# Performance work log

Hardware: AMD Instinct MI355X
Metric: run time of the kernel (lower is better)

Reference implementation:

```python
import jax, jax.numpy as jnp
import numpy as np


def _pad_reflect_br(x):
    # kornia filter2d with a 2x2 kernel pads (0 before, 1 after) in H and W, reflect mode
    return jnp.pad(x, ((0, 1), (0, 1)), mode='reflect')


def _gx(img):
    # correlation with [[-1,1],[-1,1]] at 'same' positions (pad after only)
    p = _pad_reflect_br(img)
    return -p[:-1, :-1] + p[:-1, 1:] - p[1:, :-1] + p[1:, 1:]


def _gy(img):
    # correlation with [[-1,-1],[1,1]]
    p = _pad_reflect_br(img)
    return -p[:-1, :-1] - p[:-1, 1:] + p[1:, :-1] + p[1:, 1:]


def _gsum(img):
    # correlation with all-ones 2x2 kernel
    p = _pad_reflect_br(img)
    return p[:-1, :-1] + p[:-1, 1:] + p[1:, :-1] + p[1:, 1:]


def _box3(x):
    # 3x3 neighborhood sum with zero padding. Zero padding exactly reproduces the
    # truncated patches the python loop sees at the bottom/right borders.
    H, W = x.shape
    p = jnp.pad(x, ((1, 1), (1, 1)))
    out = jnp.zeros_like(x)
    for i in range(3):
        for j in range(3):
            out = out + p[i:i + H, j:j + W]
    return out


def _lk_flow(image_prev, image_next):
    prev = image_prev[0, 0]
    nxt = image_next[0, 0]
    resx = 0.5 * (_gx(prev) + _gx(nxt))
    resy = 0.5 * (_gy(prev) + _gy(nxt))
    resdt = 0.5 * (-_gsum(prev) + _gsum(nxt))

    # structure tensor sums over 3x3 patches (A A^T and b A^T of the original loop)
    Sxx = _box3(resx * resx)
    Syy = _box3(resy * resy)
    Sxy = _box3(resx * resy)
    Sxt = _box3(resdt * resx)
    Syt = _box3(resdt * resy)

    det = Sxx * Syy - Sxy * Sxy
    safe_det = jnp.where(det != 0, det, jnp.ones_like(det))
    u = jnp.where(det != 0, (Syy * Sxt - Sxy * Syt) / safe_det, 0.0)
    v = jnp.where(det != 0, (Sxx * Syt - Sxy * Sxt) / safe_det, 0.0)

    # the python loop starts at i=1, j=1, so row 0 and col 0 stay zero
    u = jnp.pad(u[1:, 1:], ((1, 0), (1, 0)))
    v = jnp.pad(v[1:, 1:], ((1, 0), (1, 0)))
    return jnp.stack([u, v])[None]  # (1, 2, H, W)


def setup_inputs() -> dict:
    key = jax.random.key(0)
    k1, k2 = jax.random.split(key)
    H = W = 2048
    image_prev = jax.random.uniform(k1, (1, 1, H, W), dtype=jnp.float32)
    image_next = jax.random.uniform(k2, (1, 1, H, W), dtype=jnp.float32)
    return {"image_prev": image_prev, "image_next": image_next}


def reference(image_prev, image_next):
    return _lk_flow(image_prev, image_next)
```

## Files before the change

### kernel.cpp

```cpp
#include <hip/hip_runtime.h>


#pragma clang fp contract(off)

typedef float v2f __attribute__((ext_vector_type(2)));

#define IMG_H 2048
#define IMG_W 2048
#define TW 32
#define TH 32
#define LDSW 35

__global__ __launch_bounds__(256, 4)
void lk_flow_v6(const float* __restrict__ prev,
                const float* __restrict__ next,
                float* __restrict__ out) {
    #pragma clang fp contract(off)
    __shared__ float srx[(TH + 2) * LDSW];
    __shared__ float sry[(TH + 2) * LDSW];
    __shared__ float srt[(TH + 2) * LDSW];

    const int lin = (int)blockIdx.y * (int)gridDim.x + (int)blockIdx.x;
    const int nl  = (lin >> 3) + (lin & 7) * 512;
    const int r0  = (nl >> 6) * TH;
    const int c0  = (nl & 63) * TW;

    const int tx  = (int)threadIdx.x;
    const int ty  = (int)threadIdx.y;
    const int tid = ty * 8 + tx;

    for (int t = tid; t < (TH + 2) * 8; t += 256) {
        const int hr = t >> 3;
        const int ch = t & 7;
        const int a  = r0 - 1 + hr;
        const int b  = c0 + ch * 4;
        float rx[4], ry[4], rt[4];
        if (a >= 0 && a < IMG_H) {
            const int a1 = (a + 1 == IMG_H) ? (IMG_H - 2) : (a + 1);
            const int b4 = (b + 4 == IMG_W) ? (IMG_W - 2) : (b + 4);
            const float4 P0 = *reinterpret_cast<const float4*>(&prev[(size_t)a  * IMG_W + b]);
            const float4 P1 = *reinterpret_cast<const float4*>(&prev[(size_t)a1 * IMG_W + b]);
            const float4 Q0 = *reinterpret_cast<const float4*>(&next[(size_t)a  * IMG_W + b]);
            const float4 Q1 = *reinterpret_cast<const float4*>(&next[(size_t)a1 * IMG_W + b]);
            const v2f m[5] = { {P0.x, Q0.x}, {P0.y, Q0.y}, {P0.z, Q0.z}, {P0.w, Q0.w},
                               {prev[(size_t)a  * IMG_W + b4], next[(size_t)a  * IMG_W + b4]} };
            const v2f n[5] = { {P1.x, Q1.x}, {P1.y, Q1.y}, {P1.z, Q1.z}, {P1.w, Q1.w},
                               {prev[(size_t)a1 * IMG_W + b4], next[(size_t)a1 * IMG_W + b4]} };
            #pragma unroll
            for (int k = 0; k < 4; ++k) {
                const v2f A  = m[k] + m[k + 1];
                const v2f D  = m[k + 1] - m[k];
                const v2f GX = (D - n[k]) + n[k + 1];
                const v2f GY = (n[k] - A) + n[k + 1];
                const v2f GS = (A + n[k]) + n[k + 1];
                rx[k] = 0.5f * (GX.x + GX.y);
                ry[k] = 0.5f * (GY.x + GY.y);
                rt[k] = 0.5f * (GS.y - GS.x);
            }
        } else {
            #pragma unroll
            for (int k = 0; k < 4; ++k) { rx[k] = 0.f; ry[k] = 0.f; rt[k] = 0.f; }
        }
        const int base = hr * LDSW + ch * 4;
        #pragma unroll
        for (int k = 0; k < 4; ++k) {
            srx[base + k] = rx[k];
            sry[base + k] = ry[k];
            srt[base + k] = rt[k];
        }
    }

    for (int t = tid; t < (TH + 2) * 2; t += 256) {
        const int hr = t >> 1;
        const int e  = t & 1;
        const int a  = r0 - 1 + hr;
        const int bc = e ? (c0 + TW) : (c0 - 1);
        const int lc = e ? 32 : 33;
        float rx = 0.f, ry = 0.f, rt = 0.f;
        if (a >= 0 && a < IMG_H && bc >= 0 && bc < IMG_W) {
            const int a1 = (a + 1 == IMG_H) ? (IMG_H - 2) : (a + 1);
            const int b1 = (bc + 1 == IMG_W) ? (IMG_W - 2) : (bc + 1);
            const v2f m0 = { prev[(size_t)a  * IMG_W + bc], next[(size_t)a  * IMG_W + bc] };
            const v2f m1 = { prev[(size_t)a  * IMG_W + b1], next[(size_t)a  * IMG_W + b1] };
            const v2f n0 = { prev[(size_t)a1 * IMG_W + bc], next[(size_t)a1 * IMG_W + bc] };
            const v2f n1 = { prev[(size_t)a1 * IMG_W + b1], next[(size_t)a1 * IMG_W + b1] };
            const v2f A  = m0 + m1;
            const v2f D  = m1 - m0;
            const v2f GX = (D - n0) + n1;
            const v2f GY = (n0 - A) + n1;
            const v2f GS = (A + n0) + n1;
            rx = 0.5f * (GX.x + GX.y);
            ry = 0.5f * (GY.x + GY.y);
            rt = 0.5f * (GS.y - GS.x);
        }
        const int o = hr * LDSW + lc;
        srx[o] = rx; sry[o] = ry; srt[o] = rt;
    }

    __syncthreads();

    const int jb  = tx * 4;
    const int cm1 = (tx == 0) ? 33 : (jb - 1);

    const float* px = srx + ty * LDSW;
    const float* py = sry + ty * LDSW;
    const float* pt = srt + ty * LDSW;

    v2f accA[4], accB[4];
    float accC[4];
    #pragma unroll
    for (int q = 0; q < 4; ++q) { accA[q] = (v2f){0.f, 0.f}; accB[q] = (v2f){0.f, 0.f}; accC[q] = 0.f; }

    #pragma unroll 1
    for (int rr = 0; rr < 3; ++rr) {
        const float X[6] = { px[cm1], px[jb], px[jb+1], px[jb+2], px[jb+3], px[jb+4] };
        const float Y[6] = { py[cm1], py[jb], py[jb+1], py[jb+2], py[jb+3], py[jb+4] };
        const float T[6] = { pt[cm1], pt[jb], pt[jb+1], pt[jb+2], pt[jb+3], pt[jb+4] };
        px += LDSW; py += LDSW; pt += LDSW;
        v2f PA[6], PB[6];
        float PC[6];
        #pragma unroll
        for (int k = 0; k < 6; ++k) {
            const v2f xy = { X[k], Y[k] };
            PA[k] = xy * xy;
            const v2f xt = { X[k], T[k] };
            const v2f yx = { Y[k], X[k] };
            PB[k] = xt * yx;
            PC[k] = T[k] * Y[k];
        }
        #pragma unroll
        for (int q = 0; q < 4; ++q) {
            accA[q] += PA[q]; accA[q] += PA[q + 1]; accA[q] += PA[q + 2];
            accB[q] += PB[q]; accB[q] += PB[q + 1]; accB[q] += PB[q + 2];
            accC[q] += PC[q]; accC[q] += PC[q + 1]; accC[q] += PC[q + 2];
        }
    }

    const int i = r0 + ty;
    float uo[4], vo[4];
    #pragma unroll
    for (int q = 0; q < 4; ++q) {
        const float Sxx = accA[q].x, Syy = accA[q].y;
        const float Sxy = accB[q].x, Sxt = accB[q].y;
        const float Syt = accC[q];
        const float t1 = Sxx * Syy;
        const float t2 = Sxy * Sxy;
        const float det = t1 - t2;
        float u = 0.f, v = 0.f;
        if (det != 0.f) {
            const float inv = __builtin_amdgcn_rcpf(det);
            const float n1 = Syy * Sxt - Sxy * Syt;
            const float n2 = Sxx * Syt - Sxy * Sxt;
            u = n1 * inv;
            v = n2 * inv;
        }
        const int j = c0 + jb + q;
        if (i == 0 || j == 0) { u = 0.f; v = 0.f; }
        uo[q] = u; vo[q] = v;
    }
    float4 U = {uo[0], uo[1], uo[2], uo[3]};
    float4 V = {vo[0], vo[1], vo[2], vo[3]};
    *reinterpret_cast<float4*>(&out[(size_t)i * IMG_W + (c0 + jb)]) = U;
    *reinterpret_cast<float4*>(&out[(size_t)(IMG_H + i) * IMG_W + (c0 + jb)]) = V;
}

extern "C" void kernel_launch(void* const* d_in, const int* in_sizes, int n_in,
                              void* d_out, int out_size, void* d_ws, size_t ws_size,
                              hipStream_t stream) {
    const float* prev = (const float*)d_in[0];
    const float* next = (const float*)d_in[1];
    float* out = (float*)d_out;
    dim3 grid(IMG_W / TW, IMG_H / TH);
    dim3 block(8, 32);
    lk_flow_v6<<<grid, block, 0, stream>>>(prev, next, out);
}
```

Before: 25.93 us.

## Split interior tiles onto a branch-free fast path and shift the LDS halo layout

Adds an interior-tile fast path that drops reflect-padding and bounds checks, unrolls the staging loop into two fixed passes, and moves the left halo column to LDS column 0 so the box-filter reads are contiguous with no wrap index. Border tiles fall back to a generic per-pixel loop. The packed v2f arithmetic is replaced with scalar float ops, index math switches to 32-bit ints, and the 3-row accumulation loop is fully unrolled. The aim is to cut divergence, address arithmetic and instruction count, at the cost of a slower border path and possibly higher register pressure from the unrolled loop.

```diff
diff --git a/kernel.cpp b/kernel.cpp
--- a/kernel.cpp
+++ b/kernel.cpp
@@ -2,8 +2,6 @@
 
 
 #pragma clang fp contract(off)
-
-typedef float v2f __attribute__((ext_vector_type(2)));
 
 #define IMG_H 2048
 #define IMG_W 2048
@@ -12,7 +10,7 @@
 #define LDSW 35
 
 __global__ __launch_bounds__(256, 4)
-void lk_flow_v6(const float* __restrict__ prev,
+void lk_flow_v7(const float* __restrict__ prev,
                 const float* __restrict__ next,
                 float* __restrict__ out) {
     #pragma clang fp contract(off)
@@ -29,110 +27,132 @@
     const int ty  = (int)threadIdx.y;
     const int tid = ty * 8 + tx;
 
-    for (int t = tid; t < (TH + 2) * 8; t += 256) {
-        const int hr = t >> 3;
-        const int ch = t & 7;
-        const int a  = r0 - 1 + hr;
-        const int b  = c0 + ch * 4;
-        float rx[4], ry[4], rt[4];
-        if (a >= 0 && a < IMG_H) {
-            const int a1 = (a + 1 == IMG_H) ? (IMG_H - 2) : (a + 1);
-            const int b4 = (b + 4 == IMG_W) ? (IMG_W - 2) : (b + 4);
-            const float4 P0 = *reinterpret_cast<const float4*>(&prev[(size_t)a  * IMG_W + b]);
-            const float4 P1 = *reinterpret_cast<const float4*>(&prev[(size_t)a1 * IMG_W + b]);
-            const float4 Q0 = *reinterpret_cast<const float4*>(&next[(size_t)a  * IMG_W + b]);
-            const float4 Q1 = *reinterpret_cast<const float4*>(&next[(size_t)a1 * IMG_W + b]);
-            const v2f m[5] = { {P0.x, Q0.x}, {P0.y, Q0.y}, {P0.z, Q0.z}, {P0.w, Q0.w},
-                               {prev[(size_t)a  * IMG_W + b4], next[(size_t)a  * IMG_W + b4]} };
-            const v2f n[5] = { {P1.x, Q1.x}, {P1.y, Q1.y}, {P1.z, Q1.z}, {P1.w, Q1.w},
-                               {prev[(size_t)a1 * IMG_W + b4], next[(size_t)a1 * IMG_W + b4]} };
-            #pragma unroll
-            for (int k = 0; k < 4; ++k) {
-                const v2f A  = m[k] + m[k + 1];
-                const v2f D  = m[k + 1] - m[k];
-                const v2f GX = (D - n[k]) + n[k + 1];
-                const v2f GY = (n[k] - A) + n[k + 1];
-                const v2f GS = (A + n[k]) + n[k + 1];
-                rx[k] = 0.5f * (GX.x + GX.y);
-                ry[k] = 0.5f * (GY.x + GY.y);
-                rt[k] = 0.5f * (GS.y - GS.x);
+    const bool interior = (r0 > 0) & (r0 + TH + 2 <= IMG_H - 1) &
+                          (c0 > 0) & (c0 + TW + 2 <= IMG_W - 1);
+
+    if (interior) {
+        #pragma unroll
+        for (int pass = 0; pass < 2; ++pass) {
+            const int t = tid + pass * 256;
+            if (pass == 0 || tid < 16) {
+                const int hr = t >> 3;
+                const int ch = t & 7;
+                const int i0 = (r0 - 1 + hr) * IMG_W + (c0 + ch * 4);
+                const int i1 = i0 + IMG_W;
+                const float4 P0 = *reinterpret_cast<const float4*>(prev + i0);
+                const float4 P1 = *reinterpret_cast<const float4*>(prev + i1);
+                const float4 Q0 = *reinterpret_cast<const float4*>(next + i0);
+                const float4 Q1 = *reinterpret_cast<const float4*>(next + i1);
+                const float p0[5] = {P0.x, P0.y, P0.z, P0.w, prev[i0 + 4]};
+                const float p1[5] = {P1.x, P1.y, P1.z, P1.w, prev[i1 + 4]};
+                const float q0[5] = {Q0.x, Q0.y, Q0.z, Q0.w, next[i0 + 4]};
+                const float q1[5] = {Q1.x, Q1.y, Q1.z, Q1.w, next[i1 + 4]};
+                const int base = hr * LDSW + 1 + ch * 4;
+                #pragma unroll
+                for (int k = 0; k < 4; ++k) {
+                    const float Ap = p0[k] + p0[k + 1];
+                    const float Aq = q0[k] + q0[k + 1];
+                    const float gxp = ((p0[k + 1] - p0[k]) - p1[k]) + p1[k + 1];
+                    const float gxq = ((q0[k + 1] - q0[k]) - q1[k]) + q1[k + 1];
+                    const float gyp = (p1[k] - Ap) + p1[k + 1];
+                    const float gyq = (q1[k] - Aq) + q1[k + 1];
+                    const float gsp = (Ap + p1[k]) + p1[k + 1];
+                    const float gsq = (Aq + q1[k]) + q1[k + 1];
+                    srx[base + k] = 0.5f * (gxp + gxq);
+                    sry[base + k] = 0.5f * (gyp + gyq);
+                    srt[base + k] = 0.5f * (gsq - gsp);
+                }
             }
-        } else {
-            #pragma unroll
-            for (int k = 0; k < 4; ++k) { rx[k] = 0.f; ry[k] = 0.f; rt[k] = 0.f; }
         }
-        const int base = hr * LDSW + ch * 4;
-        #pragma unroll
-        for (int k = 0; k < 4; ++k) {
-            srx[base + k] = rx[k];
-            sry[base + k] = ry[k];
-            srt[base + k] = rt[k];
+        if (tid < 68) {
+            const int hr = tid >> 1;
+            const int e  = tid & 1;
+            const int bc = e ? (c0 + TW) : (c0 - 1);
+            const int i0 = (r0 - 1 + hr) * IMG_W + bc;
+            const int i1 = i0 + IMG_W;
+            const float p00 = prev[i0], p01 = prev[i0 + 1];
+            const float p10 = prev[i1], p11 = prev[i1 + 1];
+            const float q00 = next[i0], q01 = next[i0 + 1];
+            const float q10 = next[i1], q11 = next[i1 + 1];
+            const float Ap = p00 + p01, Aq = q00 + q01;
+            const float gxp = ((p01 - p00) - p10) + p11;
+            const float gxq = ((q01 - q00) - q10) + q11;
+            const float gyp = (p10 - Ap) + p11;
+            const float gyq = (q10 - Aq) + q11;
+            const float gsp = (Ap + p10) + p11;
+            const float gsq = (Aq + q10) + q11;
+            const int o = hr * LDSW + (e ? 33 : 0);
+            srx[o] = 0.5f * (gxp + gxq);
+            sry[o] = 0.5f * (gyp + gyq);
+            srt[o] = 0.5f * (gsq - gsp);
         }
-    }
-
-    for (int t = tid; t < (TH + 2) * 2; t += 256) {
-        const int hr = t >> 1;
-        const int e  = t & 1;
-        const int a  = r0 - 1 + hr;
-        const int bc = e ? (c0 + TW) : (c0 - 1);
-        const int lc = e ? 32 : 33;
-        float rx = 0.f, ry = 0.f, rt = 0.f;
-        if (a >= 0 && a < IMG_H && bc >= 0 && bc < IMG_W) {
-            const int a1 = (a + 1 == IMG_H) ? (IMG_H - 2) : (a + 1);
-            const int b1 = (bc + 1 == IMG_W) ? (IMG_W - 2) : (bc + 1);
-            const v2f m0 = { prev[(size_t)a  * IMG_W + bc], next[(size_t)a  * IMG_W + bc] };
-            const v2f m1 = { prev[(size_t)a  * IMG_W + b1], next[(size_t)a  * IMG_W + b1] };
-            const v2f n0 = { prev[(size_t)a1 * IMG_W + bc], next[(size_t)a1 * IMG_W + bc] };
-            const v2f n1 = { prev[(size_t)a1 * IMG_W + b1], next[(size_t)a1 * IMG_W + b1] };
-            const v2f A  = m0 + m1;
-            const v2f D  = m1 - m0;
-            const v2f GX = (D - n0) + n1;
-            const v2f GY = (n0 - A) + n1;
-            const v2f GS = (A + n0) + n1;
-            rx = 0.5f * (GX.x + GX.y);
-            ry = 0.5f * (GY.x + GY.y);
-            rt = 0.5f * (GS.y - GS.x);
+    } else {
+        for (int t = tid; t < 34 * 34; t += 256) {
+            const int hr = t / 34;
+            const int c  = t - hr * 34;
+            const int a  = r0 - 1 + hr;
+            const int bc = c0 - 1 + c;
+            float rx = 0.f, ry = 0.f, rt = 0.f;
+            if (a >= 0 && a < IMG_H && bc >= 0 && bc < IMG_W) {
+                const int a1 = (a + 1 == IMG_H) ? (IMG_H - 2) : (a + 1);
+                const int b1 = (bc + 1 == IMG_W) ? (IMG_W - 2) : (bc + 1);
+                const int i0 = a * IMG_W, i1 = a1 * IMG_W;
+                const float p00 = prev[i0 + bc], p01 = prev[i0 + b1];
+                const float p10 = prev[i1 + bc], p11 = prev[i1 + b1];
+                const float q00 = next[i0 + bc], q01 = next[i0 + b1];
+                const float q10 = next[i1 + bc], q11 = next[i1 + b1];
+                const float Ap = p00 + p01, Aq = q00 + q01;
+                const float gxp = ((p01 - p00) - p10) + p11;
+                const float gxq = ((q01 - q00) - q10) + q11;
+                const float gyp = (p10 - Ap) + p11;
+                const float gyq = (q10 - Aq) + q11;
+                const float gsp = (Ap + p10) + p11;
+                const float gsq = (Aq + q10) + q11;
+                rx = 0.5f * (gxp + gxq);
+                ry = 0.5f * (gyp + gyq);
+                rt = 0.5f * (gsq - gsp);
+            }
+            const int o = hr * LDSW + c;
+            srx[o] = rx; sry[o] = ry; srt[o] = rt;
         }
-        const int o = hr * LDSW + lc;
-        srx[o] = rx; sry[o] = ry; srt[o] = rt;
     }
 
     __syncthreads();
 
-    const int jb  = tx * 4;
-    const int cm1 = (tx == 0) ? 33 : (jb - 1);
+    const int jb = tx * 4;
+    int off = ty * LDSW + jb;
 
-    const float* px = srx + ty * LDSW;
-    const float* py = sry + ty * LDSW;
-    const float* pt = srt + ty * LDSW;
+    float aXX[4] = {0.f, 0.f, 0.f, 0.f};
+    float aYY[4] = {0.f, 0.f, 0.f, 0.f};
+    float aXY[4] = {0.f, 0.f, 0.f, 0.f};
+    float aXT[4] = {0.f, 0.f, 0.f, 0.f};
+    float aYT[4] = {0.f, 0.f, 0.f, 0.f};
 
-    v2f accA[4], accB[4];
-    float accC[4];
     #pragma unroll
-    for (int q = 0; q < 4; ++q) { accA[q] = (v2f){0.f, 0.f}; accB[q] = (v2f){0.f, 0.f}; accC[q] = 0.f; }
-
-    #pragma unroll 1
     for (int rr = 0; rr < 3; ++rr) {
-        const float X[6] = { px[cm1], px[jb], px[jb+1], px[jb+2], px[jb+3], px[jb+4] };
-        const float Y[6] = { py[cm1], py[jb], py[jb+1], py[jb+2], py[jb+3], py[jb+4] };
-        const float T[6] = { pt[cm1], pt[jb], pt[jb+1], pt[jb+2], pt[jb+3], pt[jb+4] };
-        px += LDSW; py += LDSW; pt += LDSW;
-        v2f PA[6], PB[6];
-        float PC[6];
+        const float* px = srx + off;
+        const float* py = sry + off;
+        const float* pt = srt + off;
+        float X[6], Y[6], T[6];
+        #pragma unroll
+        for (int k = 0; k < 6; ++k) { X[k] = px[k]; Y[k] = py[k]; T[k] = pt[k]; }
+        off += LDSW;
+        float xx[6], yy[6], xy[6], xt[6], yt[6];
         #pragma unroll
         for (int k = 0; k < 6; ++k) {
-            const v2f xy = { X[k], Y[k] };
-            PA[k] = xy * xy;
-            const v2f xt = { X[k], T[k] };
-            const v2f yx = { Y[k], X[k] };
-            PB[k] = xt * yx;
-            PC[k] = T[k] * Y[k];
+            xx[k] = X[k] * X[k];
+            yy[k] = Y[k] * Y[k];
+            xy[k] = X[k] * Y[k];
+            xt[k] = T[k] * X[k];
+            yt[k] = T[k] * Y[k];
         }
         #pragma unroll
         for (int q = 0; q < 4; ++q) {
-            accA[q] += PA[q]; accA[q] += PA[q + 1]; accA[q] += PA[q + 2];
-            accB[q] += PB[q]; accB[q] += PB[q + 1]; accB[q] += PB[q + 2];
-            accC[q] += PC[q]; accC[q] += PC[q + 1]; accC[q] += PC[q + 2];
+            aXX[q] += xx[q]; aXX[q] += xx[q + 1]; aXX[q] += xx[q + 2];
+            aYY[q] += yy[q]; aYY[q] += yy[q + 1]; aYY[q] += yy[q + 2];
+            aXY[q] += xy[q]; aXY[q] += xy[q + 1]; aXY[q] += xy[q + 2];
+            aXT[q] += xt[q]; aXT[q] += xt[q + 1]; aXT[q] += xt[q + 2];
+            aYT[q] += yt[q]; aYT[q] += yt[q + 1]; aYT[q] += yt[q + 2];
         }
     }
 
@@ -140,9 +160,8 @@
     float uo[4], vo[4];
     #pragma unroll
     for (int q = 0; q < 4; ++q) {
-        const float Sxx = accA[q].x, Syy = accA[q].y;
-        const float Sxy = accB[q].x, Sxt = accB[q].y;
-        const float Syt = accC[q];
+        const float Sxx = aXX[q], Syy = aYY[q], Sxy = aXY[q];
+        const float Sxt = aXT[q], Syt = aYT[q];
         const float t1 = Sxx * Syy;
         const float t2 = Sxy * Sxy;
         const float det = t1 - t2;
@@ -158,10 +177,11 @@
         if (i == 0 || j == 0) { u = 0.f; v = 0.f; }
         uo[q] = u; vo[q] = v;
     }
+    const int oidx = i * IMG_W + (c0 + jb);
     float4 U = {uo[0], uo[1], uo[2], uo[3]};
     float4 V = {vo[0], vo[1], vo[2], vo[3]};
-    *reinterpret_cast<float4*>(&out[(size_t)i * IMG_W + (c0 + jb)]) = U;
-    *reinterpret_cast<float4*>(&out[(size_t)(IMG_H + i) * IMG_W + (c0 + jb)]) = V;
+    *reinterpret_cast<float4*>(out + oidx) = U;
+    *reinterpret_cast<float4*>(out + IMG_H * IMG_W + oidx) = V;
 }
 
 extern "C" void kernel_launch(void* const* d_in, const int* in_sizes, int n_in,
@@ -172,5 +192,5 @@
     float* out = (float*)d_out;
     dim3 grid(IMG_W / TW, IMG_H / TH);
     dim3 block(8, 32);
-    lk_flow_v6<<<grid, block, 0, stream>>>(prev, next, out);
+    lk_flow_v7<<<grid, block, 0, stream>>>(prev, next, out);
 }
```

After: 24.38 us. 6.0% less time.
